# Kernel optimization log

Measured on AMD Instinct MI355X. Metric: run time of the kernel, lower is better.

Reference implementation:

```python
import jax, jax.numpy as jnp
import numpy as np

B = 32; NMAX = 256; E = 512; H = 512; U = 256; M = 32; L = 2; P = 4; TAU = 1.0
S = NMAX + 1                      # pseudo-seq len = nodes + SOS
IN0 = E + (M - 1) + P             # GRU layer-0 input size


def setup_inputs() -> dict:
    key = jax.random.key(0)
    ks = jax.random.split(key, 22)
    f = lambda k, sh, sc=0.05: jax.random.normal(k, sh, dtype=jnp.float32) * sc
    return {
        "h_padded": jax.random.normal(ks[0], (B, NMAX, E), jnp.float32),
        "hg": jax.random.normal(ks[1], (B, E), jnp.float32),
        "num_nodes": jax.random.randint(ks[2], (B,), 1, NMAX + 1),
        "u_noise": jax.random.uniform(ks[3], (M, B, S), jnp.float32),
        "emb_special": f(ks[4], (2, E), 1.0),
        "emb_pos": f(ks[5], (M, P), 1.0),
        "Wp": f(ks[6], (L * H, E)), "bp": f(ks[7], (L * H,)),
        "W_ih0": f(ks[8], (3 * H, IN0)), "W_hh0": f(ks[9], (3 * H, H)),
        "b_ih0": f(ks[10], (3 * H,)), "b_hh0": f(ks[11], (3 * H,)),
        "W_ih1": f(ks[12], (3 * H, H)), "W_hh1": f(ks[13], (3 * H, H)),
        "b_ih1": f(ks[14], (3 * H,)), "b_hh1": f(ks[15], (3 * H,)),
        "W1": f(ks[16], (U, H)), "W2": f(ks[17], (U, H)),
        "wc": f(ks[18], (U,)), "V": f(ks[19], (U,)),
        "Wf": f(ks[20], (M - 1, H)), "bf": f(ks[21], (M - 1,)),
    }


def _gru_step(x, hid, params):
    # torch nn.GRU single time step, L layers; gate order (r, z, n)
    new = []
    inp = x
    for l, (Wi, Wh, bi, bh) in enumerate(params):
        hp = hid[l]
        gi = inp @ Wi.T + bi
        gh = hp @ Wh.T + bh
        gi_r, gi_z, gi_n = jnp.split(gi, 3, axis=-1)
        gh_r, gh_z, gh_n = jnp.split(gh, 3, axis=-1)
        r = jax.nn.sigmoid(gi_r + gh_r)
        z = jax.nn.sigmoid(gi_z + gh_z)
        n = jnp.tanh(gi_n + r * gh_n)
        hn = (1.0 - z) * n + z * hp
        new.append(hn)
        inp = hn
    return inp, jnp.stack(new, 0)


def reference(h_padded, hg, num_nodes, u_noise, emb_special, emb_pos, Wp, bp,
              W_ih0, W_hh0, b_ih0, b_hh0, W_ih1, W_hh1, b_ih1, b_hh1,
              W1, W2, wc, V, Wf, bf):
    lens = num_nodes + 1
    mask = jnp.arange(S)[None, :] < lens[:, None]                       # [B,S]
    node_valid = (jnp.arange(NMAX)[None, :] < num_nodes[:, None]).astype(h_padded.dtype)
    # encoder_out = [SOS emb ; h nodes ; zero pad] as pad_sequence would give
    sos_enc = jnp.broadcast_to(emb_special[1], (B, 1, E))
    encoder_out = jnp.concatenate([sos_enc, h_padded * node_valid[..., None]], axis=1)  # [B,S,E]
    enc_W1 = encoder_out @ W1.T                                          # [B,S,U] hoisted (loop-invariant)
    dec_hidden = jnp.tanh(hg @ Wp.T + bp).reshape(B, L, H).transpose(1, 0, 2)  # [L,B,H]
    theta0 = jnp.zeros((B, M - 1), encoder_out.dtype)
    dec_input = jnp.concatenate([jnp.broadcast_to(emb_special[0], (B, E)), theta0], axis=1)
    cov_vec0 = jnp.zeros((B, S), encoder_out.dtype)
    gumbel = -jnp.log(-jnp.log(u_noise + 1e-10) + 1e-10)                 # [M,B,S]
    gru_params = ((W_ih0, W_hh0, b_ih0, b_hh0), (W_ih1, W_hh1, b_ih1, b_hh1))
    neg = jnp.float32(-1e30)

    def step(carry, xs):
        dec_in, hid, cov_vec, cov_loss = carry
        i, pe, g = xs
        x = jnp.concatenate([dec_in, jnp.broadcast_to(pe, (B, P))], axis=1)
        out, hid = _gru_step(x, hid, gru_params)                        # out [B,H]
        # Bahdanau attention with coverage
        uj = enc_W1 + (out @ W2.T)[:, None, :] + cov_vec[..., None] * wc
        uj = jnp.tanh(uj) @ V                                           # [B,S]
        aj = jax.nn.softmax(jnp.where(mask, uj, neg), axis=-1)
        # hard gumbel-softmax (straight-through)
        logits = jnp.log(aj + 1e-12)
        y = jax.nn.softmax((logits + g) / TAU, axis=1)
        onehot = jax.nn.one_hot(jnp.argmax(y, axis=1), S, dtype=y.dtype)
        hard = jax.lax.stop_gradient(onehot - y) + y
        chosen = jnp.einsum('bse,bs->be', encoder_out, hard)            # [B,E]
        cov_loss = cov_loss + jnp.minimum(aj, cov_vec).sum()
        cov_vec = cov_vec + aj
        theta = jnp.where(i < 1,
                          jnp.zeros((B, M - 1), out.dtype),
                          jax.nn.sigmoid(out @ Wf.T + bf))
        dec_next = jnp.concatenate([chosen, theta], axis=1)
        return (dec_next, hid, cov_vec, cov_loss), (hard, theta, aj)

    init = (dec_input, dec_hidden, cov_vec0, jnp.float32(0.0))
    xs = (jnp.arange(M), emb_pos, gumbel)
    carry_f, (hards, thetas, ajs) = jax.lax.scan(step, init, xs)
    cov_loss = carry_f[3] / B
    pointer = jnp.transpose(hards, (1, 2, 0))   # [B,S,M]
    adj = jnp.transpose(thetas, (1, 2, 0))      # [B,M-1,M]
    atts = jnp.transpose(ajs, (1, 2, 0))        # [B,S,M]
    return pointer, cov_loss, encoder_out, adj, atts
```

## Files before the change

### kernel.cpp

```cpp
#include <hip/hip_runtime.h>

constexpr int NB  = 32;
constexpr int NMX = 256;
constexpr int ED  = 512;
constexpr int HD  = 512;
constexpr int UD  = 256;
constexpr int MS  = 32;
constexpr int PD  = 4;
constexpr int SD  = 257;
constexpr int IL0 = 547;
constexpr int XP  = 576;

constexpr long long OFF_PTR  = 0;
constexpr long long OFF_COVL = (long long)NB*SD*MS;
constexpr long long OFF_ENC  = OFF_COVL + 1;
constexpr long long OFF_ADJ  = OFF_ENC + (long long)NB*SD*ED;
constexpr long long OFF_ATT  = OFF_ADJ + (long long)NB*(MS-1)*MS;

__device__ __forceinline__ float sigf(float x){ return 1.0f/(1.0f + __expf(-x)); }
__device__ __forceinline__ float ftanh(float x){ float e = __expf(2.0f*x); return 1.0f - 2.0f/(e + 1.0f); }

__global__ __launch_bounds__(256) void k_init(const float* __restrict__ hp,
                      const float* __restrict__ hg,
                      const float* __restrict__ embsp, const float* __restrict__ embpos,
                      const float* __restrict__ W1, const float* __restrict__ Wih0,
                      const float* __restrict__ W2, const int* __restrict__ nn,
                      float* __restrict__ out, float* __restrict__ x4,
                      float* __restrict__ hg4,
                      float* __restrict__ cov, float* __restrict__ covl,
                      float* __restrict__ W1T, float* __restrict__ Wih0_4,
                      float* __restrict__ W2T){
  int blk = blockIdx.x, t = threadIdx.x;
  {
    int r = blk*2 + (t >> 7);
    int tid = t & 127;
    int b = r / SD, s = r % SD;
    float* dst = out + OFF_ENC + (long long)r*ED + tid*4;
    if (s == 0){
      const float* src = embsp + ED + tid*4;
      dst[0] = src[0]; dst[1] = src[1]; dst[2] = src[2]; dst[3] = src[3];
    } else if (s-1 < nn[b]){
      const float* src = hp + ((long long)b*NMX + (s-1))*ED + tid*4;
      float4 v = *(const float4*)src;
      dst[0] = v.x; dst[1] = v.y; dst[2] = v.z; dst[3] = v.w;
    } else {
      dst[0] = 0.f; dst[1] = 0.f; dst[2] = 0.f; dst[3] = 0.f;
    }
  }
  const int N0 = XP*NB;
  const int N1 = N0 + ED*NB;
  const int N2 = N1 + NB*SD;
  const int N3 = N2 + NB;
  const int N4 = N3 + UD*ED;
  const int N5 = N4 + 1536*XP;
  const int N6 = N5 + ED*UD;
  for (int i = blk*256 + t; i < N6; i += 4112*256){
    if (i < N0){
      int kb = i >> 7, r = i & 3;
      int k = kb*4 + r;
      float v;
      if (k < ED) v = embsp[k];
      else if (k < ED + MS - 1) v = 0.f;
      else if (k < IL0) v = embpos[k - (ED + MS - 1)];
      else v = 0.f;
      x4[i] = v;
    } else if (i < N1){
      int j = i - N0;
      int kb = j >> 7, b = (j >> 2) & 31, r = j & 3;
      hg4[j] = hg[(long long)b*ED + kb*4 + r];
    } else if (i < N2){
      cov[i - N1] = 0.f;
    } else if (i < N3){
      covl[i - N2] = 0.f;
    } else if (i < N4){
      int j = i - N3; int k = j / UD, u = j % UD;
      W1T[j] = W1[(long long)u*ED + k];
    } else if (i < N5){
      int j = i - N4; int row = j / XP, c = j % XP;
      Wih0_4[j] = (c < IL0) ? Wih0[(long long)row*IL0 + c] : 0.f;
    } else {
      int j = i - N5; int k = j / UD, u = j % UD;
      W2T[j] = W2[(long long)u*HD + k];
    }
  }
}

__global__ __launch_bounds__(256) void k_ew1h(const float* __restrict__ out,
                        const float4* __restrict__ W1T4, float4* __restrict__ encW1,
                        const float4* __restrict__ hg4, const float4* __restrict__ Wp4,
                        const float* __restrict__ bp, float* __restrict__ h0,
                        float* __restrict__ h1){
  __shared__ __align__(16) float As[16][68];
  __shared__ __align__(16) float Bs[16][68];
  int blk = blockIdx.x, t = threadIdx.x;
  if (blk < 516){
    int bm = blk >> 2, bn = blk & 3;
    int m0 = bm*64, n0 = bn*64;
    const float* A = out + OFF_ENC;
    int tm = t >> 4, tn = t & 15;
    float4 acc[4];
    #pragma unroll
    for (int i = 0; i < 4; ++i) acc[i] = {0.f,0.f,0.f,0.f};
    int arow = t >> 2, akq = t & 3;
    int bk = t >> 4, bnq = t & 15;
    for (int k0 = 0; k0 < 512; k0 += 16){
      float av[4];
      bool okA = (m0 + arow) < NB*SD;
      long long abase = (long long)(m0 + arow)*ED + k0 + akq*4;
      #pragma unroll
      for (int j = 0; j < 4; ++j) av[j] = okA ? A[abase + j] : 0.f;
      float4 bv = W1T4[(long long)(k0 + bk)*64 + (n0 >> 2) + bnq];
      __syncthreads();
      #pragma unroll
      for (int j = 0; j < 4; ++j) As[akq*4 + j][arow] = av[j];
      *(float4*)&Bs[bk][bnq*4] = bv;
      __syncthreads();
      #pragma unroll
      for (int kk = 0; kk < 16; ++kk){
        float4 a = *(const float4*)&As[kk][tm*4];
        float4 bq = *(const float4*)&Bs[kk][tn*4];
        acc[0].x += a.x*bq.x; acc[0].y += a.x*bq.y; acc[0].z += a.x*bq.z; acc[0].w += a.x*bq.w;
        acc[1].x += a.y*bq.x; acc[1].y += a.y*bq.y; acc[1].z += a.y*bq.z; acc[1].w += a.y*bq.w;
        acc[2].x += a.z*bq.x; acc[2].y += a.z*bq.y; acc[2].z += a.z*bq.z; acc[2].w += a.z*bq.w;
        acc[3].x += a.w*bq.x; acc[3].y += a.w*bq.y; acc[3].z += a.w*bq.z; acc[3].w += a.w*bq.w;
      }
    }
    #pragma unroll
    for (int i = 0; i < 4; ++i){
      int r = m0 + tm*4 + i;
      if (r < NB*SD) encW1[(long long)r*64 + (n0 >> 2) + tn] = acc[i];
    }
  } else {
    int b = t & 31;
    int row = (blk - 516)*8 + (t >> 5);
    const float4* w = Wp4 + (long long)row*128;
    float acc = bp[row];
    #pragma unroll 4
    for (int i = 0; i < 128; ++i){
      float4 wv = w[i], xv = hg4[i*NB + b];
      acc += wv.x*xv.x + wv.y*xv.y + wv.z*xv.z + wv.w*xv.w;
    }
    float v = ftanh(acc);
    int h = row & 511;
    int idx = (h >> 2)*128 + b*4 + (h & 3);
    if (row < HD) h0[idx] = v;
    else          h1[idx] = v;
  }
}

template<int PER>
__global__ __launch_bounds__(512) void k_gru(const float4* __restrict__ x4,
                      const float4* __restrict__ h4,
                      const float4* __restrict__ Wih4, const float4* __restrict__ Whh4,
                      const float* __restrict__ bih, const float* __restrict__ bhh,
                      float* __restrict__ outT){
  constexpr int NI4 = PER*8;
  __shared__ float part[2][NB][8][6];
  int t = threadIdx.x;
  int b = t & 31, ks = (t >> 5) & 7, hl = (t >> 8) & 1;
  int h = blockIdx.x*2 + hl;
  float ai0 = 0.f, ai1 = 0.f, ai2 = 0.f, ah0 = 0.f, ah1 = 0.f, ah2 = 0.f;
  {
    const float4* w0 = Wih4 + (long long)(0*HD + h)*NI4 + ks*PER;
    const float4* w1 = Wih4 + (long long)(1*HD + h)*NI4 + ks*PER;
    const float4* w2 = Wih4 + (long long)(2*HD + h)*NI4 + ks*PER;
    const float4* xb = x4 + (long long)(ks*PER)*NB + b;
    #pragma unroll
    for (int kb = 0; kb < PER; ++kb){
      float4 xv = xb[kb*NB];
      float4 a = w0[kb], c = w1[kb], d = w2[kb];
      ai0 += xv.x*a.x + xv.y*a.y + xv.z*a.z + xv.w*a.w;
      ai1 += xv.x*c.x + xv.y*c.y + xv.z*c.z + xv.w*c.w;
      ai2 += xv.x*d.x + xv.y*d.y + xv.z*d.z + xv.w*d.w;
    }
  }
  {
    const float4* w0 = Whh4 + (long long)(0*HD + h)*128 + ks*16;
    const float4* w1 = Whh4 + (long long)(1*HD + h)*128 + ks*16;
    const float4* w2 = Whh4 + (long long)(2*HD + h)*128 + ks*16;
    const float4* hb = h4 + (long long)(ks*16)*NB + b;
    #pragma unroll
    for (int kb = 0; kb < 16; ++kb){
      float4 xv = hb[kb*NB];
      float4 a = w0[kb], c = w1[kb], d = w2[kb];
      ah0 += xv.x*a.x + xv.y*a.y + xv.z*a.z + xv.w*a.w;
      ah1 += xv.x*c.x + xv.y*c.y + xv.z*c.z + xv.w*c.w;
      ah2 += xv.x*d.x + xv.y*d.y + xv.z*d.z + xv.w*d.w;
    }
  }
  part[hl][b][ks][0] = ai0; part[hl][b][ks][1] = ai1; part[hl][b][ks][2] = ai2;
  part[hl][b][ks][3] = ah0; part[hl][b][ks][4] = ah1; part[hl][b][ks][5] = ah2;
  __syncthreads();
  if (t < 64){
    int b2 = t & 31, hl2 = t >> 5;
    int h2 = blockIdx.x*2 + hl2;
    float g0=0.f,g1=0.f,g2=0.f,g3=0.f,g4=0.f,g5=0.f;
    #pragma unroll
    for (int k = 0; k < 8; ++k){
      g0 += part[hl2][b2][k][0]; g1 += part[hl2][b2][k][1]; g2 += part[hl2][b2][k][2];
      g3 += part[hl2][b2][k][3]; g4 += part[hl2][b2][k][4]; g5 += part[hl2][b2][k][5];
    }
    float gir = g0 + bih[h2], giz = g1 + bih[HD + h2], gin = g2 + bih[2*HD + h2];
    float ghr = g3 + bhh[h2], ghz = g4 + bhh[HD + h2], ghn = g5 + bhh[2*HD + h2];
    float r = sigf(gir + ghr);
    float z = sigf(giz + ghz);
    float nn = ftanh(gin + r*ghn);
    int idx = (h2 >> 2)*128 + b2*4 + (h2 & 3);
    float hp = ((const float*)h4)[idx];
    outT[idx] = (1.f - z)*nn + z*hp;
  }
}

__global__ __launch_bounds__(512) void k_qs(const float4* __restrict__ h1,
                      const float4* __restrict__ W2T4, const float4* __restrict__ Wf4,
                      const float* __restrict__ bfv, const float* __restrict__ embpos,
                      int m, const float4* __restrict__ encW1,
                      const float4* __restrict__ wc4, const float4* __restrict__ V4,
                      const int* __restrict__ nn,
                      const float* __restrict__ cov, float* __restrict__ sc,
                      float* __restrict__ x4, float* __restrict__ out){
  __shared__ __align__(16) float h1s[512];
  __shared__ __align__(16) float wcs[256];
  __shared__ __align__(16) float Vs[256];
  __shared__ __align__(16) float qs[256];
  __shared__ __align__(16) float4 qpart[8][64];
  int t = threadIdx.x;
  int b = blockIdx.x >> 2, seg = blockIdx.x & 3;
  int n = nn[b];
  if (seg != 0 && seg*65 > n) return;
  if (t < 128) ((float4*)h1s)[t] = h1[t*NB + b];
  else if (t < 192) ((float4*)wcs)[t - 128] = wc4[t - 128];
  else if (t < 256) ((float4*)Vs)[t - 192] = V4[t - 192];
  __syncthreads();
  {
    int u4 = t & 63, kq = t >> 6;
    float4 acc = {0.f,0.f,0.f,0.f};
    const float4* w = W2T4 + (long long)(kq*64)*64 + u4;
    const float* hh = h1s + kq*64;
    #pragma unroll 4
    for (int k = 0; k < 64; ++k){
      float a = hh[k];
      float4 wv = w[(long long)k*64];
      acc.x += a*wv.x; acc.y += a*wv.y; acc.z += a*wv.z; acc.w += a*wv.w;
    }
    qpart[kq][u4] = acc;
  }
  __syncthreads();
  if (t < 64){
    float4 s = qpart[0][t];
    #pragma unroll
    for (int k = 1; k < 8; ++k){
      float4 p = qpart[k][t];
      s.x += p.x; s.y += p.y; s.z += p.z; s.w += p.w;
    }
    ((float4*)qs)[t] = s;
  } else if (seg == 0){
    int w = (t >> 6) - 1;
    int lane = t & 63;
    for (int j = w; j < MS-1; j += 7){
      const float4* wf = Wf4 + (long long)j*128 + lane*2;
      float4 w0 = wf[0], w1v = wf[1];
      const float4* hh4 = (const float4*)h1s + lane*2;
      float4 hv0 = hh4[0], hv1 = hh4[1];
      float d = w0.x*hv0.x + w0.y*hv0.y + w0.z*hv0.z + w0.w*hv0.w
              + w1v.x*hv1.x + w1v.y*hv1.y + w1v.z*hv1.z + w1v.w*hv1.w;
      for (int off = 32; off; off >>= 1) d += __shfl_xor(d, off);
      if (lane == 0){
        float th = (m < 1) ? 0.f : sigf(d + bfv[j]);
        out[OFF_ADJ + (long long)b*(MS-1)*MS + (long long)j*MS + m] = th;
        int k = ED + j;
        x4[(k >> 2)*128 + b*4 + (k & 3)] = th;
      }
    }
  }
  if (seg == 0 && t == 0 && m + 1 < MS){
    #pragma unroll
    for (int p = 0; p < PD; ++p){
      int k = ED + MS - 1 + p;
      x4[(k >> 2)*128 + b*4 + (k & 3)] = embpos[(m+1)*PD + p];
    }
  }
  __syncthreads();
  int lane = t & 63, wav = t >> 6;
  int s0 = seg*65;
  float4 q4 = ((const float4*)qs)[lane];
  float4 wv = ((const float4*)wcs)[lane];
  float4 vv = ((const float4*)Vs)[lane];
  for (int s = s0 + wav; s < s0 + 65 && s < SD; s += 8){
    if (s > n) continue;
    float cv = cov[b*SD + s];
    float4 e4 = encW1[((long long)b*SD + s)*64 + lane];
    float acc = vv.x*ftanh(e4.x + q4.x + cv*wv.x)
              + vv.y*ftanh(e4.y + q4.y + cv*wv.y)
              + vv.z*ftanh(e4.z + q4.z + cv*wv.z)
              + vv.w*ftanh(e4.w + q4.w + cv*wv.w);
    for (int off = 32; off; off >>= 1) acc += __shfl_xor(acc, off);
    if (lane == 0) sc[b*SD + s] = acc;
  }
}

__global__ __launch_bounds__(512) void k_soft(const float* __restrict__ sc,
                      const int* __restrict__ nn, const float* __restrict__ un, int m,
                      float* __restrict__ cov, float* __restrict__ covl,
                      float* __restrict__ out, float4* __restrict__ x4,
                      const float* __restrict__ enc){
  __shared__ float red[8]; __shared__ float redc[8]; __shared__ int redi[8];
  __shared__ float s_mx, s_den; __shared__ int s_k;
  int b = blockIdx.x, t = threadIdx.x;
  int lane = t & 63, wav = t >> 6;
  int n = nn[b];
  float sv = (t < SD) ? sc[b*SD + t] : -3.4e38f;
  float cv = (t < SD) ? cov[b*SD + t] : 0.f;
  float v1 = (t < SD && t <= n) ? sv : -3.4e38f;
  for (int off = 32; off; off >>= 1) v1 = fmaxf(v1, __shfl_xor(v1, off));
  if (lane == 0) red[wav] = v1;
  __syncthreads();
  if (t == 0){
    float mm = red[0];
    for (int i = 1; i < 8; ++i) mm = fmaxf(mm, red[i]);
    s_mx = mm;
  }
  __syncthreads();
  float ev = (t < SD && t <= n) ? __expf(sv - s_mx) : 0.f;
  float v2 = ev;
  for (int off = 32; off; off >>= 1) v2 += __shfl_xor(v2, off);
  if (lane == 0) red[wav] = v2;
  __syncthreads();
  if (t == 0){
    float ss = 0.f;
    for (int i = 0; i < 8; ++i) ss += red[i];
    s_den = ss;
  }
  __syncthreads();
  float aj = (t < SD) ? ev / s_den : 0.f;
  float yl = -3.4e38f; int idx = SD; float lcl = 0.f;
  if (t < SD){
    float u = un[((long long)m*NB + b)*SD + t];
    float g = -__logf(-__logf(u + 1e-10f) + 1e-10f);
    yl = __logf(aj + 1e-12f) + g;
    idx = t;
    lcl = fminf(aj, cv);
    cov[b*SD + t] = cv + aj;
    out[OFF_ATT + ((long long)b*SD + t)*MS + m] = aj;
  }
  for (int off = 32; off; off >>= 1){
    float oy = __shfl_xor(yl, off); int oi = __shfl_xor(idx, off);
    if (oy > yl || (oy == yl && oi < idx)){ yl = oy; idx = oi; }
  }
  for (int off = 32; off; off >>= 1) lcl += __shfl_xor(lcl, off);
  if (lane == 0){ red[wav] = yl; redi[wav] = idx; redc[wav] = lcl; }
  __syncthreads();
  if (t == 0){
    float by = red[0]; int bi = redi[0]; float cl = redc[0];
    for (int w = 1; w < 8; ++w){
      if (red[w] > by || (red[w] == by && redi[w] < bi)){ by = red[w]; bi = redi[w]; }
      cl += redc[w];
    }
    s_k = bi;
    covl[b] += cl;
  }
  __syncthreads();
  int kk = s_k;
  if (t < SD) out[OFF_PTR + ((long long)b*SD + t)*MS + m] = (t == kk) ? 1.f : 0.f;
  const float* er = enc + ((long long)b*SD + kk)*ED;
  if (t < 128){
    float4 v; v.x = er[t*4]; v.y = er[t*4+1]; v.z = er[t*4+2]; v.w = er[t*4+3];
    x4[t*NB + b] = v;
  }
}

__global__ void k_fin(const float* __restrict__ covl, float* __restrict__ out){
  if (threadIdx.x == 0 && blockIdx.x == 0){
    float s = 0.f;
    for (int i = 0; i < NB; ++i) s += covl[i];
    out[OFF_COVL] = s / (float)NB;
  }
}

extern "C" void kernel_launch(void* const* d_in, const int* in_sizes, int n_in,
                              void* d_out, int out_size, void* d_ws, size_t ws_size,
                              hipStream_t stream){
  const float* h_padded    = (const float*)d_in[0];
  const float* hg          = (const float*)d_in[1];
  const int*   num_nodes   = (const int*)  d_in[2];
  const float* u_noise     = (const float*)d_in[3];
  const float* emb_special = (const float*)d_in[4];
  const float* emb_pos     = (const float*)d_in[5];
  const float* Wp          = (const float*)d_in[6];
  const float* bp          = (const float*)d_in[7];
  const float* W_ih0       = (const float*)d_in[8];
  const float* W_hh0       = (const float*)d_in[9];
  const float* b_ih0       = (const float*)d_in[10];
  const float* b_hh0       = (const float*)d_in[11];
  const float* W_ih1       = (const float*)d_in[12];
  const float* W_hh1       = (const float*)d_in[13];
  const float* b_ih1       = (const float*)d_in[14];
  const float* b_hh1       = (const float*)d_in[15];
  const float* W1          = (const float*)d_in[16];
  const float* W2          = (const float*)d_in[17];
  const float* wc          = (const float*)d_in[18];
  const float* V           = (const float*)d_in[19];
  const float* Wf          = (const float*)d_in[20];
  const float* bf          = (const float*)d_in[21];
  float* out = (float*)d_out;

  float* ws      = (float*)d_ws;
  float* encW1   = ws;  ws += (long long)NB*SD*UD;
  float* Wih0_4  = ws;  ws += (long long)1536*XP;
  float* W1T     = ws;  ws += (long long)UD*ED;
  float* W2T     = ws;  ws += (long long)UD*ED;
  float* x4      = ws;  ws += XP*NB;
  float* hg4     = ws;  ws += ED*NB;
  float* h0      = ws;  ws += 2*HD*NB;
  float* h1      = ws;  ws += 2*HD*NB;
  float* cov     = ws;  ws += NB*SD;
  float* covl    = ws;  ws += NB;
  float* sc      = ws;  ws += NB*SD;

  k_init<<<4112, 256, 0, stream>>>(h_padded, hg, emb_special, emb_pos, W1, W_ih0, W2,
                                   num_nodes, out, x4, hg4, cov, covl, W1T, Wih0_4, W2T);
  k_ew1h<<<644, 256, 0, stream>>>(out, (const float4*)W1T, (float4*)encW1,
                                  (const float4*)hg4, (const float4*)Wp, bp, h0, h1);

  for (int m = 0; m < MS; ++m){
    float* h0c = h0 + (m & 1)*HD*NB;
    float* h0n = h0 + ((m + 1) & 1)*HD*NB;
    float* h1c = h1 + (m & 1)*HD*NB;
    float* h1n = h1 + ((m + 1) & 1)*HD*NB;
    k_gru<18><<<256, 512, 0, stream>>>((const float4*)x4, (const float4*)h0c,
        (const float4*)Wih0_4, (const float4*)W_hh0, b_ih0, b_hh0, h0n);
    k_gru<16><<<256, 512, 0, stream>>>((const float4*)h0n, (const float4*)h1c,
        (const float4*)W_ih1, (const float4*)W_hh1, b_ih1, b_hh1, h1n);
    k_qs  <<<128, 512, 0, stream>>>((const float4*)h1n, (const float4*)W2T,
        (const float4*)Wf, bf, emb_pos, m, (const float4*)encW1,
        (const float4*)wc, (const float4*)V, num_nodes, cov, sc, x4, out);
    k_soft<<<NB, 512, 0, stream>>>(sc, num_nodes, u_noise, m, cov, covl, out,
        (float4*)x4, out + OFF_ENC);
  }
  k_fin<<<1, 64, 0, stream>>>(covl, out);
}
```

Measured before the change: 1.378 ms.

## Split-K the encoder W1 GEMM and double k_qs block count per batch

The encoder-by-W1 GEMM is split along K into two halves that write separate buffers, and a new reduction kernel sums them, provided the workspace is large enough. This doubles the block count to fill more compute units. Separately, k_qs now uses 8 segments of 33 positions per batch instead of 4 of 65, launching 256 blocks to spread the attention-score work. In exchange, the split adds an extra kernel and a full read-write pass over encW1, and each k_qs block redundantly recomputes the query projection, now 8 times per batch.

```diff
diff --git a/kernel.cpp b/kernel.cpp
--- a/kernel.cpp
+++ b/kernel.cpp
@@ -85,6 +85,65 @@
   }
 }
 
+__device__ __forceinline__ void gemm_tile(const float* __restrict__ A,
+                      const float4* __restrict__ W1T4, float4* __restrict__ dst,
+                      int m0, int n0, int k0b, int k0e, int t,
+                      float (*As)[68], float (*Bs)[68]){
+  int tm = t >> 4, tn = t & 15;
+  float4 acc[4];
+  #pragma unroll
+  for (int i = 0; i < 4; ++i) acc[i] = {0.f,0.f,0.f,0.f};
+  int arow = t >> 2, akq = t & 3;
+  int bk = t >> 4, bnq = t & 15;
+  for (int k0 = k0b; k0 < k0e; k0 += 16){
+    float av[4];
+    bool okA = (m0 + arow) < NB*SD;
+    long long abase = (long long)(m0 + arow)*ED + k0 + akq*4;
+    #pragma unroll
+    for (int j = 0; j < 4; ++j) av[j] = okA ? A[abase + j] : 0.f;
+    float4 bv = W1T4[(long long)(k0 + bk)*64 + (n0 >> 2) + bnq];
+    __syncthreads();
+    #pragma unroll
+    for (int j = 0; j < 4; ++j) As[akq*4 + j][arow] = av[j];
+    *(float4*)&Bs[bk][bnq*4] = bv;
+    __syncthreads();
+    #pragma unroll
+    for (int kk = 0; kk < 16; ++kk){
+      float4 a = *(const float4*)&As[kk][tm*4];
+      float4 bq = *(const float4*)&Bs[kk][tn*4];
+      acc[0].x += a.x*bq.x; acc[0].y += a.x*bq.y; acc[0].z += a.x*bq.z; acc[0].w += a.x*bq.w;
+      acc[1].x += a.y*bq.x; acc[1].y += a.y*bq.y; acc[1].z += a.y*bq.z; acc[1].w += a.y*bq.w;
+      acc[2].x += a.z*bq.x; acc[2].y += a.z*bq.y; acc[2].z += a.z*bq.z; acc[2].w += a.z*bq.w;
+      acc[3].x += a.w*bq.x; acc[3].y += a.w*bq.y; acc[3].z += a.w*bq.z; acc[3].w += a.w*bq.w;
+    }
+  }
+  #pragma unroll
+  for (int i = 0; i < 4; ++i){
+    int r = m0 + tm*4 + i;
+    if (r < NB*SD) dst[(long long)r*64 + (n0 >> 2) + tm*0 + (t & 15)] = acc[i];
+  }
+}
+
+__device__ __forceinline__ void hid0_body(int blk0, int blk, int t,
+                      const float4* __restrict__ hg4, const float4* __restrict__ Wp4,
+                      const float* __restrict__ bp, float* __restrict__ h0,
+                      float* __restrict__ h1){
+  int b = t & 31;
+  int row = (blk - blk0)*8 + (t >> 5);
+  const float4* w = Wp4 + (long long)row*128;
+  float acc = bp[row];
+  #pragma unroll 4
+  for (int i = 0; i < 128; ++i){
+    float4 wv = w[i], xv = hg4[i*NB + b];
+    acc += wv.x*xv.x + wv.y*xv.y + wv.z*xv.z + wv.w*xv.w;
+  }
+  float v = ftanh(acc);
+  int h = row & 511;
+  int idx = (h >> 2)*128 + b*4 + (h & 3);
+  if (row < HD) h0[idx] = v;
+  else          h1[idx] = v;
+}
+
 __global__ __launch_bounds__(256) void k_ew1h(const float* __restrict__ out,
                         const float4* __restrict__ W1T4, float4* __restrict__ encW1,
                         const float4* __restrict__ hg4, const float4* __restrict__ Wp4,
@@ -94,57 +153,37 @@
   __shared__ __align__(16) float Bs[16][68];
   int blk = blockIdx.x, t = threadIdx.x;
   if (blk < 516){
-    int bm = blk >> 2, bn = blk & 3;
-    int m0 = bm*64, n0 = bn*64;
-    const float* A = out + OFF_ENC;
-    int tm = t >> 4, tn = t & 15;
-    float4 acc[4];
-    #pragma unroll
-    for (int i = 0; i < 4; ++i) acc[i] = {0.f,0.f,0.f,0.f};
-    int arow = t >> 2, akq = t & 3;
-    int bk = t >> 4, bnq = t & 15;
-    for (int k0 = 0; k0 < 512; k0 += 16){
-      float av[4];
-      bool okA = (m0 + arow) < NB*SD;
-      long long abase = (long long)(m0 + arow)*ED + k0 + akq*4;
-      #pragma unroll
-      for (int j = 0; j < 4; ++j) av[j] = okA ? A[abase + j] : 0.f;
-      float4 bv = W1T4[(long long)(k0 + bk)*64 + (n0 >> 2) + bnq];
-      __syncthreads();
-      #pragma unroll
-      for (int j = 0; j < 4; ++j) As[akq*4 + j][arow] = av[j];
-      *(float4*)&Bs[bk][bnq*4] = bv;
-      __syncthreads();
-      #pragma unroll
-      for (int kk = 0; kk < 16; ++kk){
-        float4 a = *(const float4*)&As[kk][tm*4];
-        float4 bq = *(const float4*)&Bs[kk][tn*4];
-        acc[0].x += a.x*bq.x; acc[0].y += a.x*bq.y; acc[0].z += a.x*bq.z; acc[0].w += a.x*bq.w;
-        acc[1].x += a.y*bq.x; acc[1].y += a.y*bq.y; acc[1].z += a.y*bq.z; acc[1].w += a.y*bq.w;
-        acc[2].x += a.z*bq.x; acc[2].y += a.z*bq.y; acc[2].z += a.z*bq.z; acc[2].w += a.z*bq.w;
-        acc[3].x += a.w*bq.x; acc[3].y += a.w*bq.y; acc[3].z += a.w*bq.z; acc[3].w += a.w*bq.w;
-      }
-    }
-    #pragma unroll
-    for (int i = 0; i < 4; ++i){
-      int r = m0 + tm*4 + i;
-      if (r < NB*SD) encW1[(long long)r*64 + (n0 >> 2) + tn] = acc[i];
-    }
+    gemm_tile(out + OFF_ENC, W1T4, encW1, (blk >> 2)*64, (blk & 3)*64, 0, 512, t, As, Bs);
   } else {
-    int b = t & 31;
-    int row = (blk - 516)*8 + (t >> 5);
-    const float4* w = Wp4 + (long long)row*128;
-    float acc = bp[row];
-    #pragma unroll 4
-    for (int i = 0; i < 128; ++i){
-      float4 wv = w[i], xv = hg4[i*NB + b];
-      acc += wv.x*xv.x + wv.y*xv.y + wv.z*xv.z + wv.w*xv.w;
-    }
-    float v = ftanh(acc);
-    int h = row & 511;
-    int idx = (h >> 2)*128 + b*4 + (h & 3);
-    if (row < HD) h0[idx] = v;
-    else          h1[idx] = v;
+    hid0_body(516, blk, t, hg4, Wp4, bp, h0, h1);
+  }
+}
+
+__global__ __launch_bounds__(256) void k_ew1h_ks(const float* __restrict__ out,
+                        const float4* __restrict__ W1T4, float4* __restrict__ encW1,
+                        float4* __restrict__ encP,
+                        const float4* __restrict__ hg4, const float4* __restrict__ Wp4,
+                        const float* __restrict__ bp, float* __restrict__ h0,
+                        float* __restrict__ h1){
+  __shared__ __align__(16) float As[16][68];
+  __shared__ __align__(16) float Bs[16][68];
+  int blk = blockIdx.x, t = threadIdx.x;
+  if (blk < 1032){
+    int bm = blk >> 3, bn = (blk >> 1) & 3, kh = blk & 1;
+    float4* dst = kh ? encP : encW1;
+    gemm_tile(out + OFF_ENC, W1T4, dst, bm*64, bn*64, kh*256, kh*256 + 256, t, As, Bs);
+  } else {
+    hid0_body(1032, blk, t, hg4, Wp4, bp, h0, h1);
+  }
+}
+
+__global__ __launch_bounds__(256) void k_red(float4* __restrict__ encW1,
+                                             const float4* __restrict__ encP){
+  const int N = (int)((long long)NB*SD*UD/4);
+  for (int i = blockIdx.x*256 + threadIdx.x; i < N; i += 1028*256){
+    float4 a = encW1[i], b = encP[i];
+    a.x += b.x; a.y += b.y; a.z += b.z; a.w += b.w;
+    encW1[i] = a;
   }
 }
 
@@ -225,9 +264,9 @@
   __shared__ __align__(16) float qs[256];
   __shared__ __align__(16) float4 qpart[8][64];
   int t = threadIdx.x;
-  int b = blockIdx.x >> 2, seg = blockIdx.x & 3;
+  int b = blockIdx.x >> 3, seg = blockIdx.x & 7;
   int n = nn[b];
-  if (seg != 0 && seg*65 > n) return;
+  if (seg != 0 && seg*33 > n) return;
   if (t < 128) ((float4*)h1s)[t] = h1[t*NB + b];
   else if (t < 192) ((float4*)wcs)[t - 128] = wc4[t - 128];
   else if (t < 256) ((float4*)Vs)[t - 192] = V4[t - 192];
@@ -282,11 +321,11 @@
   }
   __syncthreads();
   int lane = t & 63, wav = t >> 6;
-  int s0 = seg*65;
+  int s0 = seg*33;
   float4 q4 = ((const float4*)qs)[lane];
   float4 wv = ((const float4*)wcs)[lane];
   float4 vv = ((const float4*)Vs)[lane];
-  for (int s = s0 + wav; s < s0 + 65 && s < SD; s += 8){
+  for (int s = s0 + wav; s < s0 + 33 && s < SD; s += 8){
     if (s > n) continue;
     float cv = cov[b*SD + s];
     float4 e4 = encW1[((long long)b*SD + s)*64 + lane];
@@ -416,11 +455,21 @@
   float* cov     = ws;  ws += NB*SD;
   float* covl    = ws;  ws += NB;
   float* sc      = ws;  ws += NB*SD;
+  float* encP    = ws;
+  size_t used_base  = (size_t)((char*)ws - (char*)d_ws);
+  bool   ksplit = (ws_size >= used_base + (size_t)NB*SD*UD*sizeof(float));
 
   k_init<<<4112, 256, 0, stream>>>(h_padded, hg, emb_special, emb_pos, W1, W_ih0, W2,
                                    num_nodes, out, x4, hg4, cov, covl, W1T, Wih0_4, W2T);
-  k_ew1h<<<644, 256, 0, stream>>>(out, (const float4*)W1T, (float4*)encW1,
-                                  (const float4*)hg4, (const float4*)Wp, bp, h0, h1);
+  if (ksplit){
+    k_ew1h_ks<<<1160, 256, 0, stream>>>(out, (const float4*)W1T, (float4*)encW1,
+                                        (float4*)encP, (const float4*)hg4,
+                                        (const float4*)Wp, bp, h0, h1);
+    k_red<<<1028, 256, 0, stream>>>((float4*)encW1, (const float4*)encP);
+  } else {
+    k_ew1h<<<644, 256, 0, stream>>>(out, (const float4*)W1T, (float4*)encW1,
+                                    (const float4*)hg4, (const float4*)Wp, bp, h0, h1);
+  }
 
   for (int m = 0; m < MS; ++m){
     float* h0c = h0 + (m & 1)*HD*NB;
@@ -431,7 +480,7 @@
         (const float4*)Wih0_4, (const float4*)W_hh0, b_ih0, b_hh0, h0n);
     k_gru<16><<<256, 512, 0, stream>>>((const float4*)h0n, (const float4*)h1c,
         (const float4*)W_ih1, (const float4*)W_hh1, b_ih1, b_hh1, h1n);
-    k_qs  <<<128, 512, 0, stream>>>((const float4*)h1n, (const float4*)W2T,
+    k_qs  <<<256, 512, 0, stream>>>((const float4*)h1n, (const float4*)W2T,
         (const float4*)Wf, bf, emb_pos, m, (const float4*)encW1,
         (const float4*)wc, (const float4*)V, num_nodes, cov, sc, x4, out);
     k_soft<<<NB, 512, 0, stream>>>(sc, num_nodes, u_noise, m, cov, covl, out,
```

Result: faster. 1.289 ms (-6.5%).

## Fuse attention score and gumbel-softmax kernels via per-batch atomic flag handoff

Applied to the files above, without the earlier changes.

Merges the score kernel and the softmax/selection kernel into one launch. Each batch row is split across 8 segment blocks, and after writing its scores each block bumps a per-step atomic counter. Segment 0 spins until all 8 have arrived, then does the softmax, argmax and coverage update. This removes one kernel launch per decoder step (32 in total) and doubles the number of blocks doing score work. In exchange it relies on all blocks being co-resident: 256 blocks of 512 threads must be scheduled together, or the spin-wait can deadlock.

```diff
diff --git a/kernel.cpp b/kernel.cpp
--- a/kernel.cpp
+++ b/kernel.cpp
@@ -29,7 +29,7 @@
                       float* __restrict__ hg4,
                       float* __restrict__ cov, float* __restrict__ covl,
                       float* __restrict__ W1T, float* __restrict__ Wih0_4,
-                      float* __restrict__ W2T){
+                      float* __restrict__ W2T, int* __restrict__ flags){
   int blk = blockIdx.x, t = threadIdx.x;
   {
     int r = blk*2 + (t >> 7);
@@ -54,7 +54,8 @@
   const int N4 = N3 + UD*ED;
   const int N5 = N4 + 1536*XP;
   const int N6 = N5 + ED*UD;
-  for (int i = blk*256 + t; i < N6; i += 4112*256){
+  const int N7 = N6 + MS*NB;
+  for (int i = blk*256 + t; i < N7; i += 4112*256){
     if (i < N0){
       int kb = i >> 7, r = i & 3;
       int k = kb*4 + r;
@@ -78,9 +79,11 @@
     } else if (i < N5){
       int j = i - N4; int row = j / XP, c = j % XP;
       Wih0_4[j] = (c < IL0) ? Wih0[(long long)row*IL0 + c] : 0.f;
-    } else {
+    } else if (i < N6){
       int j = i - N5; int k = j / UD, u = j % UD;
       W2T[j] = W2[(long long)u*HD + k];
+    } else {
+      flags[i - N6] = 0;
     }
   }
 }
@@ -211,23 +214,31 @@
   }
 }
 
-__global__ __launch_bounds__(512) void k_qs(const float4* __restrict__ h1,
+__global__ __launch_bounds__(512) void k_attn(const float4* __restrict__ h1,
                       const float4* __restrict__ W2T4, const float4* __restrict__ Wf4,
                       const float* __restrict__ bfv, const float* __restrict__ embpos,
                       int m, const float4* __restrict__ encW1,
                       const float4* __restrict__ wc4, const float4* __restrict__ V4,
-                      const int* __restrict__ nn,
-                      const float* __restrict__ cov, float* __restrict__ sc,
-                      float* __restrict__ x4, float* __restrict__ out){
+                      const int* __restrict__ nn, const float* __restrict__ un,
+                      float* __restrict__ cov, float* __restrict__ covl,
+                      float* __restrict__ sc, float* __restrict__ x4,
+                      float* __restrict__ out, const float* __restrict__ enc,
+                      int* __restrict__ flag){
   __shared__ __align__(16) float h1s[512];
   __shared__ __align__(16) float wcs[256];
   __shared__ __align__(16) float Vs[256];
   __shared__ __align__(16) float qs[256];
   __shared__ __align__(16) float4 qpart[8][64];
+  __shared__ float red[8]; __shared__ float redc[8]; __shared__ int redi[8];
+  __shared__ float s_mx, s_den; __shared__ int s_k;
   int t = threadIdx.x;
-  int b = blockIdx.x >> 2, seg = blockIdx.x & 3;
+  int b = blockIdx.x >> 3, seg = blockIdx.x & 7;
   int n = nn[b];
-  if (seg != 0 && seg*65 > n) return;
+  if (seg != 0 && seg*33 > n){
+    if (t == 0)
+      __hip_atomic_fetch_add(flag + b, 1, __ATOMIC_RELEASE, __HIP_MEMORY_SCOPE_AGENT);
+    return;
+  }
   if (t < 128) ((float4*)h1s)[t] = h1[t*NB + b];
   else if (t < 192) ((float4*)wcs)[t - 128] = wc4[t - 128];
   else if (t < 256) ((float4*)Vs)[t - 192] = V4[t - 192];
@@ -281,34 +292,34 @@
     }
   }
   __syncthreads();
+  {
+    int lane = t & 63, wav = t >> 6;
+    int s0 = seg*33;
+    float4 q4 = ((const float4*)qs)[lane];
+    float4 wv = ((const float4*)wcs)[lane];
+    float4 vv = ((const float4*)Vs)[lane];
+    for (int s = s0 + wav; s < s0 + 33 && s < SD; s += 8){
+      if (s > n) continue;
+      float cv = cov[b*SD + s];
+      float4 e4 = encW1[((long long)b*SD + s)*64 + lane];
+      float acc = vv.x*ftanh(e4.x + q4.x + cv*wv.x)
+                + vv.y*ftanh(e4.y + q4.y + cv*wv.y)
+                + vv.z*ftanh(e4.z + q4.z + cv*wv.z)
+                + vv.w*ftanh(e4.w + q4.w + cv*wv.w);
+      for (int off = 32; off; off >>= 1) acc += __shfl_xor(acc, off);
+      if (lane == 0) sc[b*SD + s] = acc;
+    }
+  }
+  __syncthreads();
+  if (t == 0)
+    __hip_atomic_fetch_add(flag + b, 1, __ATOMIC_RELEASE, __HIP_MEMORY_SCOPE_AGENT);
+  if (seg != 0) return;
+  if (t == 0){
+    while (__hip_atomic_load(flag + b, __ATOMIC_RELAXED, __HIP_MEMORY_SCOPE_AGENT) < 8){}
+    (void)__hip_atomic_load(flag + b, __ATOMIC_ACQUIRE, __HIP_MEMORY_SCOPE_AGENT);
+  }
+  __syncthreads();
   int lane = t & 63, wav = t >> 6;
-  int s0 = seg*65;
-  float4 q4 = ((const float4*)qs)[lane];
-  float4 wv = ((const float4*)wcs)[lane];
-  float4 vv = ((const float4*)Vs)[lane];
-  for (int s = s0 + wav; s < s0 + 65 && s < SD; s += 8){
-    if (s > n) continue;
-    float cv = cov[b*SD + s];
-    float4 e4 = encW1[((long long)b*SD + s)*64 + lane];
-    float acc = vv.x*ftanh(e4.x + q4.x + cv*wv.x)
-              + vv.y*ftanh(e4.y + q4.y + cv*wv.y)
-              + vv.z*ftanh(e4.z + q4.z + cv*wv.z)
-              + vv.w*ftanh(e4.w + q4.w + cv*wv.w);
-    for (int off = 32; off; off >>= 1) acc += __shfl_xor(acc, off);
-    if (lane == 0) sc[b*SD + s] = acc;
-  }
-}
-
-__global__ __launch_bounds__(512) void k_soft(const float* __restrict__ sc,
-                      const int* __restrict__ nn, const float* __restrict__ un, int m,
-                      float* __restrict__ cov, float* __restrict__ covl,
-                      float* __restrict__ out, float4* __restrict__ x4,
-                      const float* __restrict__ enc){
-  __shared__ float red[8]; __shared__ float redc[8]; __shared__ int redi[8];
-  __shared__ float s_mx, s_den; __shared__ int s_k;
-  int b = blockIdx.x, t = threadIdx.x;
-  int lane = t & 63, wav = t >> 6;
-  int n = nn[b];
   float sv = (t < SD) ? sc[b*SD + t] : -3.4e38f;
   float cv = (t < SD) ? cov[b*SD + t] : 0.f;
   float v1 = (t < SD && t <= n) ? sv : -3.4e38f;
@@ -365,7 +376,7 @@
   const float* er = enc + ((long long)b*SD + kk)*ED;
   if (t < 128){
     float4 v; v.x = er[t*4]; v.y = er[t*4+1]; v.z = er[t*4+2]; v.w = er[t*4+3];
-    x4[t*NB + b] = v;
+    ((float4*)x4)[t*NB + b] = v;
   }
 }
 
@@ -416,9 +427,11 @@
   float* cov     = ws;  ws += NB*SD;
   float* covl    = ws;  ws += NB;
   float* sc      = ws;  ws += NB*SD;
+  int*   flags   = (int*)ws; ws += MS*NB;
 
   k_init<<<4112, 256, 0, stream>>>(h_padded, hg, emb_special, emb_pos, W1, W_ih0, W2,
-                                   num_nodes, out, x4, hg4, cov, covl, W1T, Wih0_4, W2T);
+                                   num_nodes, out, x4, hg4, cov, covl, W1T, Wih0_4,
+                                   W2T, flags);
   k_ew1h<<<644, 256, 0, stream>>>(out, (const float4*)W1T, (float4*)encW1,
                                   (const float4*)hg4, (const float4*)Wp, bp, h0, h1);
 
@@ -431,11 +444,10 @@
         (const float4*)Wih0_4, (const float4*)W_hh0, b_ih0, b_hh0, h0n);
     k_gru<16><<<256, 512, 0, stream>>>((const float4*)h0n, (const float4*)h1c,
         (const float4*)W_ih1, (const float4*)W_hh1, b_ih1, b_hh1, h1n);
-    k_qs  <<<128, 512, 0, stream>>>((const float4*)h1n, (const float4*)W2T,
+    k_attn<<<256, 512, 0, stream>>>((const float4*)h1n, (const float4*)W2T,
         (const float4*)Wf, bf, emb_pos, m, (const float4*)encW1,
-        (const float4*)wc, (const float4*)V, num_nodes, cov, sc, x4, out);
-    k_soft<<<NB, 512, 0, stream>>>(sc, num_nodes, u_noise, m, cov, covl, out,
-        (float4*)x4, out + OFF_ENC);
+        (const float4*)wc, (const float4*)V, num_nodes, u_noise,
+        cov, covl, sc, x4, out, out + OFF_ENC, flags + m*NB);
   }
   k_fin<<<1, 64, 0, stream>>>(covl, out);
 }
```

After: 1.459 ms. +5.9%, slower.
